# Optimization experiments

Measured on AMD Instinct MI355X. Metric: run time of the kernel, lower is better.

The kernel has to match this reference:

```python
import jax, jax.numpy as jnp
import numpy as np

EMBED_DIM = 1024
NUM_HEADS = 16
HEAD_DIM = EMBED_DIM // NUM_HEADS
LAMBDA_ENTANGLE = 0.35


def setup_inputs() -> dict:
    key = jax.random.key(0)
    ks = jax.random.split(key, 10)
    B, S, D = 2, 2048, EMBED_DIM
    init = 1.0 / np.sqrt(D)  # mimic nn.Linear uniform init scale
    x = jax.random.normal(ks[0], (B, S, D), dtype=jnp.float32)
    Wq = jax.random.uniform(ks[1], (D, D), jnp.float32, -init, init)
    bq = jax.random.uniform(ks[2], (D,), jnp.float32, -init, init)
    Wk = jax.random.uniform(ks[3], (D, D), jnp.float32, -init, init)
    bk = jax.random.uniform(ks[4], (D,), jnp.float32, -init, init)
    Wv = jax.random.uniform(ks[5], (D, D), jnp.float32, -init, init)
    bv = jax.random.uniform(ks[6], (D,), jnp.float32, -init, init)
    Wo = jax.random.uniform(ks[7], (D, D), jnp.float32, -init, init)
    bo = jax.random.uniform(ks[8], (D,), jnp.float32, -init, init)
    J_attn = jax.random.normal(ks[9], (NUM_HEADS, HEAD_DIM, HEAD_DIM), dtype=jnp.float32) * 0.02
    lambda_attn = jnp.asarray(LAMBDA_ENTANGLE, dtype=jnp.float32)
    return {"x": x, "Wq": Wq, "bq": bq, "Wk": Wk, "bk": bk, "Wv": Wv, "bv": bv,
            "Wo": Wo, "bo": bo, "J_attn": J_attn, "lambda_attn": lambda_attn}


def reference(x, Wq, bq, Wk, bk, Wv, bv, Wo, bo, J_attn, lambda_attn):
    B, S, D = x.shape
    H, Hd = NUM_HEADS, HEAD_DIM
    scale = jnp.sqrt(jnp.asarray(Hd, dtype=x.dtype))

    def heads(W, b):
        # (B,S,D) @ (D,D) + b -> (B,H,S,Hd)
        y = jnp.einsum('bsd,ed->bse', x, W) + b
        return y.reshape(B, S, H, Hd).transpose(0, 2, 1, 3)

    Q = heads(Wq, bq)
    K = heads(Wk, bk)
    V = heads(Wv, bv)

    scores = jnp.einsum('bhid,bhjd->bhij', Q, K) / scale
    # bilinear entanglement correction: tanh(Q) J tanh(K)^T
    QJ = jnp.einsum('bhid,hde->bhie', jnp.tanh(Q), J_attn)  # (B,H,S,Hd)
    delta = jnp.einsum('bhie,bhje->bhij', QJ, jnp.tanh(K))
    scores = scores + lambda_attn * delta

    causal = jnp.triu(jnp.ones((S, S), dtype=bool), k=1)
    scores = jnp.where(causal, -jnp.inf, scores)

    probs = jax.nn.softmax(scores, axis=-1)
    out = jnp.einsum('bhij,bhjd->bhid', probs, V)  # (B,H,S,Hd)
    out = out.transpose(0, 2, 1, 3).reshape(B, S, D)
    return jnp.einsum('bsd,ed->bse', out, Wo) + bo
```

## Files before the change

### kernel.cpp

```cpp
#include <hip/hip_runtime.h>
#include <hip/hip_bf16.h>

typedef unsigned short u16;
typedef __bf16 bf16x8 __attribute__((ext_vector_type(8)));
typedef float f32x4 __attribute__((ext_vector_type(4)));
typedef unsigned short u16x4 __attribute__((ext_vector_type(4)));

#define MFMA16(a, b, c) __builtin_amdgcn_mfma_f32_16x16x32_bf16(a, b, c, 0, 0, 0)

#define EMB 1024
#define SEQ 2048
#define NH 16
#define HD 64
#define LOG2E 1.4426950408889634f

#define GLOAD_LDS16(g, l) __builtin_amdgcn_global_load_lds( \
    (const __attribute__((address_space(1))) unsigned int*)(g), \
    (__attribute__((address_space(3))) unsigned int*)(l), 16, 0, 0)

__device__ __forceinline__ float b2f(u16 u) {
    union { unsigned int i; float f; } v; v.i = ((unsigned int)u) << 16; return v.f;
}
__device__ __forceinline__ u16 f2b(float f) {
    __hip_bfloat16 h = __float2bfloat16(f);
    return *reinterpret_cast<u16*>(&h);
}
__device__ __forceinline__ u16x4 pack4(float a, float b, float c, float d) {
    union { __hip_bfloat162 h2[2]; u16x4 u; } r;
    r.h2[0] = __float22bfloat162_rn(float2{a, b});
    r.h2[1] = __float22bfloat162_rn(float2{c, d});
    return r.u;
}
__device__ __forceinline__ bf16x8 ldfrag(const u16* p) {
    return *reinterpret_cast<const bf16x8*>(p);
}
__device__ __forceinline__ bf16x8 cvt8(const float* p) {
    const float4 a = *reinterpret_cast<const float4*>(p);
    const float4 b = *reinterpret_cast<const float4*>(p + 4);
    union { u16x4 q[2]; bf16x8 v; } r;
    r.q[0] = pack4(a.x, a.y, a.z, a.w);
    r.q[1] = pack4(b.x, b.y, b.z, b.w);
    return r.v;
}
__device__ __forceinline__ float fast_tanh(float x) {
    float t = __builtin_amdgcn_exp2f(x * (2.0f * LOG2E));
    return 1.0f - 2.0f * __builtin_amdgcn_rcpf(t + 1.0f);
}
__device__ __forceinline__ bf16x8 tanh8(bf16x8 v) {
    union { bf16x8 v; u16 u[8]; } in; in.v = v;
    float o[8];
#pragma unroll
    for (int e = 0; e < 8; e++) o[e] = fast_tanh(b2f(in.u[e]));
    union { u16x4 q[2]; bf16x8 v; } r;
    r.q[0] = pack4(o[0], o[1], o[2], o[3]);
    r.q[1] = pack4(o[4], o[5], o[6], o[7]);
    return r.v;
}

__global__ __launch_bounds__(256) void cvt_all(
        const float* __restrict__ x,  const float* __restrict__ Wq,
        const float* __restrict__ Wk, const float* __restrict__ Wv,
        const float* __restrict__ Wo, u16* __restrict__ dst)
{
    size_t i = ((size_t)blockIdx.x * 256 + threadIdx.x) * 8;
    const float* src; size_t off;
    if (i < 4194304) { src = x; off = i; }
    else {
        size_t j = i - 4194304; int w = (int)(j >> 20); off = j & 1048575;
        src = (w == 0) ? Wq : (w == 1) ? Wk : (w == 2) ? Wv : Wo;
    }
    *(bf16x8*)&dst[i] = cvt8(src + off);
}

template<int MI>
__global__ __launch_bounds__(256, 4) void gemm_epi(
        const u16* __restrict__ A,
        const u16* __restrict__ W0, const float* __restrict__ B0,
        const u16* __restrict__ W1, const float* __restrict__ B1,
        const u16* __restrict__ W2, const float* __restrict__ B2,
        const float* __restrict__ lam,
        u16* __restrict__ Qa, u16* __restrict__ Ka, u16* __restrict__ Vt,
        float* __restrict__ out, int modeBase)
{
    const int mode = modeBase + blockIdx.z;
    const u16* W; const float* bias;
    if (blockIdx.z == 0)      { W = W0; bias = B0; }
    else if (blockIdx.z == 1) { W = W1; bias = B1; }
    else                      { W = W2; bias = B2; }

    __shared__ __attribute__((aligned(16))) u16 sA[MI * 32 * 64];
    __shared__ __attribute__((aligned(16))) u16 sB[128 * 64];

    const int t = threadIdx.x;
    const int w = t >> 6, L = t & 63;
    const int wm = w >> 1, wn = w & 1;
    const int lr = L & 15, lq = L >> 4;
    const int wbase = t & 192;
    const int m0 = blockIdx.y * (MI * 32), n0 = blockIdx.x * 128;

    f32x4 acc[MI][4];
#pragma unroll
    for (int i = 0; i < MI; i++)
#pragma unroll
        for (int j = 0; j < 4; j++) { f32x4 z = {0.f, 0.f, 0.f, 0.f}; acc[i][j] = z; }

    for (int k0 = 0; k0 < EMB; k0 += 64) {
        __syncthreads();
#pragma unroll
        for (int q = 0; q < MI; q++) {
            int c = q * 256 + t;
            int row = c >> 3, cc = c & 7;
            int col8 = cc ^ (row & 7);
            GLOAD_LDS16(&A[(size_t)(m0 + row) * EMB + k0 + col8 * 8],
                        &sA[(q * 256 + wbase) * 8]);
        }
#pragma unroll
        for (int q = 0; q < 4; q++) {
            int c = q * 256 + t;
            int row = c >> 3, cc = c & 7;
            int col8 = cc ^ (row & 7);
            GLOAD_LDS16(&W[(size_t)(n0 + row) * EMB + k0 + col8 * 8],
                        &sB[(q * 256 + wbase) * 8]);
        }
        __syncthreads();
#pragma unroll
        for (int s = 0; s < 2; s++) {
            bf16x8 af[MI], bfr[4];
#pragma unroll
            for (int mi = 0; mi < MI; mi++) {
                int row = wm * (MI * 16) + mi * 16 + lr;
                af[mi] = ldfrag(&sA[(row * 8 + ((s * 4 + lq) ^ (row & 7))) * 8]);
            }
#pragma unroll
            for (int ni = 0; ni < 4; ni++) {
                int row = wn * 64 + ni * 16 + lr;
                bfr[ni] = ldfrag(&sB[(row * 8 + ((s * 4 + lq) ^ (row & 7))) * 8]);
            }
#pragma unroll
            for (int mi = 0; mi < MI; mi++)
#pragma unroll
                for (int ni = 0; ni < 4; ni++)
                    acc[mi][ni] = MFMA16(af[mi], bfr[ni], acc[mi][ni]);
        }
    }

    const float lamf = lam[0];
#pragma unroll
    for (int mi = 0; mi < MI; mi++)
#pragma unroll
        for (int ni = 0; ni < 4; ni++) {
            int mb = m0 + wm * (MI * 16) + mi * 16 + lq * 4;
            int n  = n0 + wn * 64 + ni * 16 + lr;
            float bv = bias[n];
            if (mode == 3) {
#pragma unroll
                for (int r = 0; r < 4; r++)
                    out[(size_t)(mb + r) * EMB + n] = acc[mi][ni][r] + bv;
            } else {
                int b = mb >> 11, s0 = mb & 2047;
                int h = n >> 6,  d = n & 63;
                if (mode == 0) {
#pragma unroll
                    for (int r = 0; r < 4; r++) {
                        float val = acc[mi][ni][r] + bv;
                        size_t i128 = ((size_t)(b * NH + h) * SEQ + s0 + r) * 128 + d;
                        Qa[i128]      = f2b(val * (0.125f * LOG2E));
                        Qa[i128 + 64] = f2b(lamf * LOG2E * fast_tanh(val));
                    }
                } else if (mode == 1) {
#pragma unroll
                    for (int r = 0; r < 4; r++) {
                        float val = acc[mi][ni][r] + bv;
                        Ka[((size_t)(b * NH + h) * SEQ + s0 + r) * 128 + d] = f2b(val);
                    }
                } else {
                    u16x4 pk = pack4(acc[mi][ni][0] + bv, acc[mi][ni][1] + bv,
                                     acc[mi][ni][2] + bv, acc[mi][ni][3] + bv);
                    *(u16x4*)&Vt[((size_t)(b * NH + h) * HD + d) * SEQ + s0] = pk;
                }
            }
        }
}

__global__ __launch_bounds__(256) void ukern(
        const float* __restrict__ J, u16* __restrict__ Ka)
{
    __shared__ __attribute__((aligned(16))) u16 sJ[64 * 72];
    const int t = threadIdx.x, w = t >> 6, L = t & 63, lr = L & 15, lq = L >> 4;
    const int rt = blockIdx.x, bh = blockIdx.y, h = bh & 15;

#pragma unroll
    for (int i = 0; i < 2; i++) {
        int c = t + 256 * i;
        int row = c >> 3, col = (c & 7) * 8;
        *(bf16x8*)&sJ[row * 72 + col] = cvt8(&J[(size_t)h * 4096 + row * 64 + col]);
    }
    __syncthreads();

    const u16* krow = &Ka[((size_t)bh * SEQ + rt * 64 + w * 16 + lr) * 128];
    bf16x8 a0 = tanh8(ldfrag(krow + lq * 8));
    bf16x8 a1 = tanh8(ldfrag(krow + lq * 8 + 32));
#pragma unroll
    for (int nt = 0; nt < 4; nt++) {
        f32x4 acc = {0.f, 0.f, 0.f, 0.f};
        acc = MFMA16(a0, ldfrag(&sJ[(nt * 16 + lr) * 72 + lq * 8]), acc);
        acc = MFMA16(a1, ldfrag(&sJ[(nt * 16 + lr) * 72 + lq * 8 + 32]), acc);
#pragma unroll
        for (int r = 0; r < 4; r++) {
            int j = rt * 64 + w * 16 + lq * 4 + r;
            Ka[((size_t)bh * SEQ + j) * 128 + 64 + nt * 16 + lr] = f2b(acc[r]);
        }
    }
}

__global__ __launch_bounds__(256) void flash(
        const u16* __restrict__ Qa, const u16* __restrict__ Ka,
        const u16* __restrict__ Vt, u16* __restrict__ attn)
{
    __shared__ __attribute__((aligned(16))) u16 sK[2][64 * 128];
    __shared__ __attribute__((aligned(16))) u16 sVt[2][64 * 64];
    __shared__ __attribute__((aligned(16))) u16 sP[128 * 72];

    const int t = threadIdx.x, w = t >> 6, L = t & 63, lr = L & 15, lq = L >> 4;
    const int bh = blockIdx.x & 31, p = blockIdx.x >> 5;
    const int qt = blockIdx.y ? 15 - p : p;
    const int qm = qt * 128;
    const int i_l = w * 16 + lr;
    const int wbase = t & 192;
    const u16* Kbase = Ka + (size_t)bh * SEQ * 128;
    const u16* Vbase = Vt + (size_t)bh * HD * SEQ;

    bf16x8 qf[2][4];
#pragma unroll
    for (int g = 0; g < 2; g++) {
        const u16* qrow = Qa + ((size_t)bh * SEQ + qm + g * 64 + i_l) * 128;
#pragma unroll
        for (int s = 0; s < 4; s++) qf[g][s] = ldfrag(qrow + s * 32 + lq * 8);
    }

    f32x4 Ot[2][4];
#pragma unroll
    for (int g = 0; g < 2; g++)
#pragma unroll
        for (int i = 0; i < 4; i++) { f32x4 z = {0.f, 0.f, 0.f, 0.f}; Ot[g][i] = z; }
    float lsum[2] = {0.f, 0.f};

    const int ktmax = 2 * qt + 1;

    auto stage = [&](int kt, int bsel) {
        const int kn = kt * 64;
#pragma unroll
        for (int q = 0; q < 4; q++) {
            int cch = q * 256 + t;
            int row = cch >> 4, cc = cch & 15;
            int col8 = cc ^ (row & 15);
            GLOAD_LDS16(&Kbase[(size_t)(kn + row) * 128 + col8 * 8],
                        &sK[bsel][(q * 256 + wbase) * 8]);
        }
#pragma unroll
        for (int q = 0; q < 2; q++) {
            int cch = q * 256 + t;
            int d = cch >> 3, cc = cch & 7;
            int j8 = cc ^ (d & 7);
            GLOAD_LDS16(&Vbase[(size_t)d * SEQ + kn + j8 * 8],
                        &sVt[bsel][(q * 256 + wbase) * 8]);
        }
    };

    stage(0, 0);
    __syncthreads();

    int cur = 0;
    for (int kt = 0; kt <= ktmax; kt++) {
        if (kt < ktmax) stage(kt + 1, cur ^ 1);
        const u16* sKc = sK[cur];
        const u16* sVc = sVt[cur];

        f32x4 sc[2][4];
#pragma unroll
        for (int g = 0; g < 2; g++)
#pragma unroll
            for (int mt = 0; mt < 4; mt++) { f32x4 z = {0.f,0.f,0.f,0.f}; sc[g][mt] = z; }
        __builtin_amdgcn_s_setprio(1);
#pragma unroll
        for (int mt = 0; mt < 4; mt++) {
            int j = mt * 16 + lr;
#pragma unroll
            for (int s = 0; s < 4; s++) {
                bf16x8 kf = ldfrag(&sKc[(j * 16 + ((s * 4 + lq) ^ (j & 15))) * 8]);
                sc[0][mt] = MFMA16(kf, qf[0][s], sc[0][mt]);
                sc[1][mt] = MFMA16(kf, qf[1][s], sc[1][mt]);
            }
        }
        __builtin_amdgcn_s_setprio(0);
        if (kt >= ktmax - 1) {
            const int thr0 = (kt == ktmax) ? -1  : i_l;
            const int thr1 = (kt == ktmax) ? i_l : 63;
#pragma unroll
            for (int mt = 0; mt < 4; mt++)
#pragma unroll
                for (int r = 0; r < 4; r++) {
                    int j = mt * 16 + lq * 4 + r;
                    if (j > thr0) sc[0][mt][r] = -INFINITY;
                    if (j > thr1) sc[1][mt][r] = -INFINITY;
                }
        }
#pragma unroll
        for (int g = 0; g < 2; g++) {
#pragma unroll
            for (int mt = 0; mt < 4; mt++)
#pragma unroll
                for (int r = 0; r < 4; r++) {
                    float e = __builtin_amdgcn_exp2f(sc[g][mt][r]);
                    sc[g][mt][r] = e;
                    lsum[g] += e;
                }
#pragma unroll
            for (int mt = 0; mt < 4; mt++)
                *(u16x4*)&sP[(g * 64 + i_l) * 72 + mt * 16 + lq * 4] =
                    pack4(sc[g][mt][0], sc[g][mt][1], sc[g][mt][2], sc[g][mt][3]);
        }
        __builtin_amdgcn_s_setprio(1);
#pragma unroll
        for (int s2 = 0; s2 < 2; s2++) {
            bf16x8 pf0 = ldfrag(&sP[(i_l) * 72 + s2 * 32 + lq * 8]);
            bf16x8 pf1 = ldfrag(&sP[(64 + i_l) * 72 + s2 * 32 + lq * 8]);
#pragma unroll
            for (int mt = 0; mt < 4; mt++) {
                int d = mt * 16 + lr;
                bf16x8 vf = ldfrag(&sVc[(d * 8 + ((s2 * 4 + lq) ^ (d & 7))) * 8]);
                Ot[0][mt] = MFMA16(vf, pf0, Ot[0][mt]);
                Ot[1][mt] = MFMA16(vf, pf1, Ot[1][mt]);
            }
        }
        __builtin_amdgcn_s_setprio(0);
        __syncthreads();
        cur ^= 1;
    }

    const int b = bh >> 4, h = bh & 15;
#pragma unroll
    for (int g = 0; g < 2; g++) {
        float ls = lsum[g];
        ls += __shfl_xor(ls, 16);
        ls += __shfl_xor(ls, 32);
        const float r0 = __builtin_amdgcn_rcpf(ls);
        const float inv = r0 * (2.0f - ls * r0);
        const size_t base = ((size_t)(b * SEQ + qm + g * 64 + i_l)) * EMB + h * HD;
#pragma unroll
        for (int mt = 0; mt < 4; mt++)
            *(u16x4*)&attn[base + mt * 16 + lq * 4] =
                pack4(Ot[g][mt][0] * inv, Ot[g][mt][1] * inv,
                      Ot[g][mt][2] * inv, Ot[g][mt][3] * inv);
    }
}

extern "C" void kernel_launch(void* const* d_in, const int* in_sizes, int n_in,
                              void* d_out, int out_size, void* d_ws, size_t ws_size,
                              hipStream_t stream)
{
    const float* x   = (const float*)d_in[0];
    const float* Wq  = (const float*)d_in[1];
    const float* bq  = (const float*)d_in[2];
    const float* Wk  = (const float*)d_in[3];
    const float* bk  = (const float*)d_in[4];
    const float* Wv  = (const float*)d_in[5];
    const float* bv  = (const float*)d_in[6];
    const float* Wo  = (const float*)d_in[7];
    const float* bo  = (const float*)d_in[8];
    const float* J   = (const float*)d_in[9];
    const float* lam = (const float*)d_in[10];

    u16* ws  = (u16*)d_ws;
    u16* xb  = ws;
    u16* Wqb = xb  + (size_t)4096 * 1024;
    u16* Wkb = Wqb + (size_t)1024 * 1024;
    u16* Wvb = Wkb + (size_t)1024 * 1024;
    u16* Wob = Wvb + (size_t)1024 * 1024;
    u16* Qa  = Wob + (size_t)1024 * 1024;
    u16* Ka  = Qa  + (size_t)32 * 2048 * 128;
    u16* Vt  = Ka  + (size_t)32 * 2048 * 128;
    u16* attn = xb;
    float* dout = (float*)d_out;

    dim3 blk(256);
    cvt_all<<<dim3(4096), blk, 0, stream>>>(x, Wq, Wk, Wv, Wo, ws);
    gemm_epi<4><<<dim3(8, 32, 3), blk, 0, stream>>>(
        xb, Wqb, bq, Wkb, bk, Wvb, bv, lam, Qa, Ka, Vt, dout, 0);
    ukern<<<dim3(32, 32), blk, 0, stream>>>(J, Ka);
    flash<<<dim3(256, 2), blk, 0, stream>>>(Qa, Ka, Vt, attn);
    gemm_epi<2><<<dim3(8, 64, 1), blk, 0, stream>>>(
        attn, Wob, bo, Wob, bo, Wob, bo, lam, Qa, Ka, Vt, dout, 3);
}
```

Baseline: 206.9 us.

## Split flash attention KV tile across two wave groups and pair causal query tiles per block

```diff
diff --git a/kernel.cpp b/kernel.cpp
--- a/kernel.cpp
+++ b/kernel.cpp
@@ -213,145 +213,168 @@
     }
 }
 
-__global__ __launch_bounds__(256) void flash(
+__global__ __launch_bounds__(512) void flash(
         const u16* __restrict__ Qa, const u16* __restrict__ Ka,
         const u16* __restrict__ Vt, u16* __restrict__ attn)
 {
     __shared__ __attribute__((aligned(16))) u16 sK[2][64 * 128];
     __shared__ __attribute__((aligned(16))) u16 sVt[2][64 * 64];
     __shared__ __attribute__((aligned(16))) u16 sP[128 * 72];
+    __shared__ float sLs[2][4][64][2];
 
     const int t = threadIdx.x, w = t >> 6, L = t & 63, lr = L & 15, lq = L >> 4;
+    const int wq = w & 3, wk = w >> 2;
     const int bh = blockIdx.x & 31, p = blockIdx.x >> 5;
-    const int qt = blockIdx.y ? 15 - p : p;
-    const int qm = qt * 128;
-    const int i_l = w * 16 + lr;
-    const int wbase = t & 192;
+    const int i_l = wq * 16 + lr;
+    const int wbase = t & 448;
     const u16* Kbase = Ka + (size_t)bh * SEQ * 128;
     const u16* Vbase = Vt + (size_t)bh * HD * SEQ;
-
-    bf16x8 qf[2][4];
-#pragma unroll
-    for (int g = 0; g < 2; g++) {
-        const u16* qrow = Qa + ((size_t)bh * SEQ + qm + g * 64 + i_l) * 128;
-#pragma unroll
-        for (int s = 0; s < 4; s++) qf[g][s] = ldfrag(qrow + s * 32 + lq * 8);
-    }
-
-    f32x4 Ot[2][4];
-#pragma unroll
-    for (int g = 0; g < 2; g++)
-#pragma unroll
-        for (int i = 0; i < 4; i++) { f32x4 z = {0.f, 0.f, 0.f, 0.f}; Ot[g][i] = z; }
-    float lsum[2] = {0.f, 0.f};
-
-    const int ktmax = 2 * qt + 1;
-
-    auto stage = [&](int kt, int bsel) {
-        const int kn = kt * 64;
-#pragma unroll
-        for (int q = 0; q < 4; q++) {
-            int cch = q * 256 + t;
+    const int b = bh >> 4, h = bh & 15;
+    float* sOt = reinterpret_cast<float*>(sK);
+
+    auto stage = [&](int kn, int bsel) {
+#pragma unroll
+        for (int q = 0; q < 2; q++) {
+            int cch = q * 512 + t;
             int row = cch >> 4, cc = cch & 15;
             int col8 = cc ^ (row & 15);
             GLOAD_LDS16(&Kbase[(size_t)(kn + row) * 128 + col8 * 8],
-                        &sK[bsel][(q * 256 + wbase) * 8]);
-        }
-#pragma unroll
-        for (int q = 0; q < 2; q++) {
-            int cch = q * 256 + t;
-            int d = cch >> 3, cc = cch & 7;
+                        &sK[bsel][(q * 512 + wbase) * 8]);
+        }
+        {
+            int d = t >> 3, cc = t & 7;
             int j8 = cc ^ (d & 7);
             GLOAD_LDS16(&Vbase[(size_t)d * SEQ + kn + j8 * 8],
-                        &sVt[bsel][(q * 256 + wbase) * 8]);
+                        &sVt[bsel][wbase * 8]);
         }
     };
 
-    stage(0, 0);
-    __syncthreads();
-
-    int cur = 0;
-    for (int kt = 0; kt <= ktmax; kt++) {
-        if (kt < ktmax) stage(kt + 1, cur ^ 1);
-        const u16* sKc = sK[cur];
-        const u16* sVc = sVt[cur];
-
-        f32x4 sc[2][4];
+#pragma unroll 1
+    for (int seg = 0; seg < 2; seg++) {
+        const int qt = seg ? 15 - p : p;
+        const int qm = qt * 128;
+        const int ktmax = 2 * qt + 1;
+
+        bf16x8 qf[2][4];
+#pragma unroll
+        for (int g = 0; g < 2; g++) {
+            const u16* qrow = Qa + ((size_t)bh * SEQ + qm + g * 64 + i_l) * 128;
+#pragma unroll
+            for (int s = 0; s < 4; s++) qf[g][s] = ldfrag(qrow + s * 32 + lq * 8);
+        }
+
+        f32x4 Ot[2][4];
 #pragma unroll
         for (int g = 0; g < 2; g++)
 #pragma unroll
-            for (int mt = 0; mt < 4; mt++) { f32x4 z = {0.f,0.f,0.f,0.f}; sc[g][mt] = z; }
-        __builtin_amdgcn_s_setprio(1);
-#pragma unroll
-        for (int mt = 0; mt < 4; mt++) {
-            int j = mt * 16 + lr;
-#pragma unroll
-            for (int s = 0; s < 4; s++) {
-                bf16x8 kf = ldfrag(&sKc[(j * 16 + ((s * 4 + lq) ^ (j & 15))) * 8]);
-                sc[0][mt] = MFMA16(kf, qf[0][s], sc[0][mt]);
-                sc[1][mt] = MFMA16(kf, qf[1][s], sc[1][mt]);
-            }
-        }
-        __builtin_amdgcn_s_setprio(0);
-        if (kt >= ktmax - 1) {
-            const int thr0 = (kt == ktmax) ? -1  : i_l;
-            const int thr1 = (kt == ktmax) ? i_l : 63;
-#pragma unroll
-            for (int mt = 0; mt < 4; mt++)
-#pragma unroll
-                for (int r = 0; r < 4; r++) {
-                    int j = mt * 16 + lq * 4 + r;
-                    if (j > thr0) sc[0][mt][r] = -INFINITY;
-                    if (j > thr1) sc[1][mt][r] = -INFINITY;
+            for (int i = 0; i < 4; i++) { f32x4 z = {0.f, 0.f, 0.f, 0.f}; Ot[g][i] = z; }
+        float lsum[2] = {0.f, 0.f};
+
+        stage(0, 0);
+        __syncthreads();
+
+        int cur = 0;
+        for (int kt = 0; kt <= ktmax; kt++) {
+            if (kt < ktmax) stage((kt + 1) * 64, cur ^ 1);
+            const u16* sKc = sK[cur];
+            const u16* sVc = sVt[cur];
+
+            f32x4 sc[2][2];
+#pragma unroll
+            for (int g = 0; g < 2; g++)
+#pragma unroll
+                for (int m = 0; m < 2; m++) { f32x4 z = {0.f,0.f,0.f,0.f}; sc[g][m] = z; }
+            __builtin_amdgcn_s_setprio(1);
+#pragma unroll
+            for (int mt2 = 0; mt2 < 2; mt2++) {
+                int j = (wk * 2 + mt2) * 16 + lr;
+#pragma unroll
+                for (int s = 0; s < 4; s++) {
+                    bf16x8 kf = ldfrag(&sKc[(j * 16 + ((s * 4 + lq) ^ (j & 15))) * 8]);
+                    sc[0][mt2] = MFMA16(kf, qf[0][s], sc[0][mt2]);
+                    sc[1][mt2] = MFMA16(kf, qf[1][s], sc[1][mt2]);
                 }
-        }
+            }
+            __builtin_amdgcn_s_setprio(0);
+            if (kt >= ktmax - 1) {
+                const int thr0 = (kt == ktmax) ? -1  : i_l;
+                const int thr1 = (kt == ktmax) ? i_l : 63;
+#pragma unroll
+                for (int mt2 = 0; mt2 < 2; mt2++)
+#pragma unroll
+                    for (int r = 0; r < 4; r++) {
+                        int j = (wk * 2 + mt2) * 16 + lq * 4 + r;
+                        if (j > thr0) sc[0][mt2][r] = -INFINITY;
+                        if (j > thr1) sc[1][mt2][r] = -INFINITY;
+                    }
+            }
+#pragma unroll
+            for (int g = 0; g < 2; g++) {
+#pragma unroll
+                for (int mt2 = 0; mt2 < 2; mt2++) {
+#pragma unroll
+                    for (int r = 0; r < 4; r++) {
+                        float e = __builtin_amdgcn_exp2f(sc[g][mt2][r]);
+                        sc[g][mt2][r] = e;
+                        lsum[g] += e;
+                    }
+                    *(u16x4*)&sP[(g * 64 + i_l) * 72 + (wk * 2 + mt2) * 16 + lq * 4] =
+                        pack4(sc[g][mt2][0], sc[g][mt2][1], sc[g][mt2][2], sc[g][mt2][3]);
+                }
+            }
+            __builtin_amdgcn_s_setprio(1);
+            {
+                bf16x8 pf0 = ldfrag(&sP[(i_l) * 72 + wk * 32 + lq * 8]);
+                bf16x8 pf1 = ldfrag(&sP[(64 + i_l) * 72 + wk * 32 + lq * 8]);
+#pragma unroll
+                for (int mt = 0; mt < 4; mt++) {
+                    int d = mt * 16 + lr;
+                    bf16x8 vf = ldfrag(&sVc[(d * 8 + ((wk * 4 + lq) ^ (d & 7))) * 8]);
+                    Ot[0][mt] = MFMA16(vf, pf0, Ot[0][mt]);
+                    Ot[1][mt] = MFMA16(vf, pf1, Ot[1][mt]);
+                }
+            }
+            __builtin_amdgcn_s_setprio(0);
+            __syncthreads();
+            cur ^= 1;
+        }
+
 #pragma unroll
         for (int g = 0; g < 2; g++) {
-#pragma unroll
-            for (int mt = 0; mt < 4; mt++)
-#pragma unroll
-                for (int r = 0; r < 4; r++) {
-                    float e = __builtin_amdgcn_exp2f(sc[g][mt][r]);
-                    sc[g][mt][r] = e;
-                    lsum[g] += e;
-                }
-#pragma unroll
-            for (int mt = 0; mt < 4; mt++)
-                *(u16x4*)&sP[(g * 64 + i_l) * 72 + mt * 16 + lq * 4] =
-                    pack4(sc[g][mt][0], sc[g][mt][1], sc[g][mt][2], sc[g][mt][3]);
-        }
-        __builtin_amdgcn_s_setprio(1);
-#pragma unroll
-        for (int s2 = 0; s2 < 2; s2++) {
-            bf16x8 pf0 = ldfrag(&sP[(i_l) * 72 + s2 * 32 + lq * 8]);
-            bf16x8 pf1 = ldfrag(&sP[(64 + i_l) * 72 + s2 * 32 + lq * 8]);
-#pragma unroll
-            for (int mt = 0; mt < 4; mt++) {
-                int d = mt * 16 + lr;
-                bf16x8 vf = ldfrag(&sVc[(d * 8 + ((s2 * 4 + lq) ^ (d & 7))) * 8]);
-                Ot[0][mt] = MFMA16(vf, pf0, Ot[0][mt]);
-                Ot[1][mt] = MFMA16(vf, pf1, Ot[1][mt]);
-            }
-        }
-        __builtin_amdgcn_s_setprio(0);
+            lsum[g] += __shfl_xor(lsum[g], 16);
+            lsum[g] += __shfl_xor(lsum[g], 32);
+            sLs[wk][wq][L][g] = lsum[g];
+        }
+        if (wk == 1) {
+            float* dst = &sOt[((size_t)wq * 64 + L) * 32];
+#pragma unroll
+            for (int g = 0; g < 2; g++)
+#pragma unroll
+                for (int mt = 0; mt < 4; mt++)
+#pragma unroll
+                    for (int r = 0; r < 4; r++)
+                        dst[g * 16 + mt * 4 + r] = Ot[g][mt][r];
+        }
         __syncthreads();
-        cur ^= 1;
-    }
-
-    const int b = bh >> 4, h = bh & 15;
-#pragma unroll
-    for (int g = 0; g < 2; g++) {
-        float ls = lsum[g];
-        ls += __shfl_xor(ls, 16);
-        ls += __shfl_xor(ls, 32);
-        const float r0 = __builtin_amdgcn_rcpf(ls);
-        const float inv = r0 * (2.0f - ls * r0);
-        const size_t base = ((size_t)(b * SEQ + qm + g * 64 + i_l)) * EMB + h * HD;
-#pragma unroll
-        for (int mt = 0; mt < 4; mt++)
-            *(u16x4*)&attn[base + mt * 16 + lq * 4] =
-                pack4(Ot[g][mt][0] * inv, Ot[g][mt][1] * inv,
-                      Ot[g][mt][2] * inv, Ot[g][mt][3] * inv);
+        if (wk == 0) {
+            const float* src = &sOt[((size_t)wq * 64 + L) * 32];
+#pragma unroll
+            for (int g = 0; g < 2; g++) {
+                float ls = lsum[g] + sLs[1][wq][L][g];
+                const float r0 = __builtin_amdgcn_rcpf(ls);
+                const float inv = r0 * (2.0f - ls * r0);
+                const size_t base =
+                    ((size_t)(b * SEQ + qm + g * 64 + i_l)) * EMB + h * HD;
+#pragma unroll
+                for (int mt = 0; mt < 4; mt++)
+                    *(u16x4*)&attn[base + mt * 16 + lq * 4] = pack4(
+                        (Ot[g][mt][0] + src[g * 16 + mt * 4 + 0]) * inv,
+                        (Ot[g][mt][1] + src[g * 16 + mt * 4 + 1]) * inv,
+                        (Ot[g][mt][2] + src[g * 16 + mt * 4 + 2]) * inv,
+                        (Ot[g][mt][3] + src[g * 16 + mt * 4 + 3]) * inv);
+            }
+        }
+        __syncthreads();
     }
 }
 
@@ -388,7 +411,7 @@
     gemm_epi<4><<<dim3(8, 32, 3), blk, 0, stream>>>(
         xb, Wqb, bq, Wkb, bk, Wvb, bv, lam, Qa, Ka, Vt, dout, 0);
     ukern<<<dim3(32, 32), blk, 0, stream>>>(J, Ka);
-    flash<<<dim3(256, 2), blk, 0, stream>>>(Qa, Ka, Vt, attn);
+    flash<<<dim3(256), dim3(512), 0, stream>>>(Qa, Ka, Vt, attn);
     gemm_epi<2><<<dim3(8, 64, 1), blk, 0, stream>>>(
         attn, Wob, bo, Wob, bo, Wob, bo, lam, Qa, Ka, Vt, dout, 3);
 }
```

Result: faster. 196.7 us (-4.9%).
